# Performance work log

Hardware: AMD Instinct MI355X
Metric: run time of the kernel (lower is better)

## Reference

```python
import jax, jax.numpy as jnp
import numpy as np

# dims: batch, q-heads, kv-heads, seq, head_dim, block size, window (kv blocks per q block)
B, H, KVH, S, D = 2, 16, 4, 4096, 64
BLK, W = 64, 8
G = H // KVH          # heads per group = 4
NQ = S // BLK         # 64 query blocks
L = W * BLK           # flattened kv window per q block = 512


def setup_inputs() -> dict:
    key = jax.random.key(0)
    k0, k1, k2, k3 = jax.random.split(key, 4)
    q = jax.random.normal(k0, (B, H, S, D), jnp.float32)
    k = jax.random.normal(k1, (B, KVH, S, D), jnp.float32)
    v = jax.random.normal(k2, (B, KVH, S, D), jnp.float32)
    # standard alibi slopes 2^(-8i/H)
    alibi_slopes = jnp.asarray(2.0 ** (-8.0 * np.arange(1, H + 1) / H), jnp.float32)
    # contiguous segments via sorted random ids
    segment_ids = jnp.sort(jax.random.randint(k3, (B, S), 0, 8, jnp.int32), axis=-1)
    # causal sliding window: q block qb attends to kv blocks [qb-W+1, qb]; -1 = invalid
    qb = np.arange(NQ)[:, None]
    bi = qb - (W - 1) + np.arange(W)[None, :]
    block_indices = jnp.asarray(np.where(bi < 0, -1, bi), jnp.int32)  # [NQ, W]
    return {"q": q, "k": k, "v": v, "alibi_slopes": alibi_slopes,
            "segment_ids": segment_ids, "block_indices": block_indices}


def reference(q, k, v, alibi_slopes, segment_ids, block_indices):
    scale = jnp.float32(1.0 / np.sqrt(D))
    NEG = jnp.float32(-1e30)

    qg = q.reshape(B, KVH, G, NQ, BLK, D)          # GQA grouping
    kb = k.reshape(B, KVH, NQ, BLK, D)
    vb = v.reshape(B, KVH, NQ, BLK, D)

    safe = jnp.clip(block_indices, 0)               # [NQ, W]
    kg = kb[:, :, safe]                             # [B,KVH,NQ,W,BLK,D] gathered kv blocks
    vg = vb[:, :, safe]

    pos_m = (jnp.arange(NQ) * BLK)[:, None] + jnp.arange(BLK)             # [NQ,BM]
    pos_n = safe[:, :, None] * BLK + jnp.arange(BLK)[None, None, :]       # [NQ,W,BN]

    valid = (block_indices >= 0)[:, None, :, None]                        # [NQ,1,W,1]
    causal = pos_m[:, :, None, None] >= pos_n[:, None, :, :]              # [NQ,BM,W,BN]
    seg_q = segment_ids.reshape(B, NQ, BLK)
    seg_k = jnp.take(segment_ids, pos_n.reshape(-1), axis=1).reshape(B, NQ, W, BLK)
    same_seg = (seg_q[:, :, :, None, None] == seg_k[:, :, None, :, :]) & (seg_q[:, :, :, None, None] >= 0)
    mask = ((valid & causal)[None] & same_seg)                            # [B,NQ,BM,W,BN]
    maskb = mask.reshape(B, 1, 1, NQ, BLK, L)                             # broadcast over KVH,G

    scores = jnp.einsum('bkgqmd,bkqwnd->bkgqmwn', qg, kg) * scale         # [B,KVH,G,NQ,BM,W,BN]
    pos_diff = jnp.abs(pos_m[:, :, None, None] - pos_n[:, None, :, :]).astype(jnp.float32)
    scores = scores - alibi_slopes.reshape(KVH, G)[None, :, :, None, None, None, None] * pos_diff
    scores = scores.reshape(B, KVH, G, NQ, BLK, L)
    scores = jnp.where(maskb, scores, NEG)

    row_max = jnp.max(scores, axis=-1, keepdims=True)
    p = jnp.where(maskb, jnp.exp(scores - row_max), 0.0)
    l = jnp.sum(p, axis=-1, keepdims=True)                                # [B,KVH,G,NQ,BM,1]
    vf = vg.reshape(B, KVH, NQ, L, D)
    acc = jnp.einsum('bkgqml,bkqld->bkgqmd', p, vf)
    out = jnp.where(l > 0, acc / jnp.where(l > 0, l, 1.0), 0.0)           # zero rows with no valid kv
    return out.reshape(B, H, S, D)
```

## Files before the change

kernel.cpp:

```cpp
#include <hip/hip_runtime.h>
#include <hip/hip_bf16.h>

#define NKVH 4
#define SEQ 4096
#define BLK 64
#define NW 8
#define NQB 64

typedef __attribute__((ext_vector_type(8))) short bf16x8;
typedef __attribute__((ext_vector_type(4))) float f32x4;

__device__ __forceinline__ unsigned pkbf(unsigned lo, unsigned hi) {
  return __builtin_amdgcn_perm(hi + 0x8000u, lo + 0x8000u, 0x07060302u);
}

__device__ __forceinline__ void gload16(const void* g, void* l) {
  __builtin_amdgcn_global_load_lds(
      (const __attribute__((address_space(1))) void*)g,
      (__attribute__((address_space(3))) void*)l, 16, 0, 0);
}

__global__ __launch_bounds__(256, 2)
void prep_kernel(const float* __restrict__ kp, const float* __restrict__ vp,
                 const int* __restrict__ seg,
                 short* __restrict__ kw, short* __restrict__ vt,
                 int* __restrict__ fo)
{
  const int ki = blockIdx.x, kvh = blockIdx.y, b = blockIdx.z;
  const size_t base = (((size_t)(b*NKVH + kvh)*SEQ) + (size_t)ki*BLK)*64;
  __shared__ float sk[64][72];
  __shared__ float sv[64][72];
  const int t = threadIdx.x;
  #pragma unroll
  for (int it = 0; it < 4; ++it) {
    const int i = t + it*256;
    const int row = i >> 4, c4 = i & 15;
    float4 a = *(const float4*)(kp + base + row*64 + c4*4);
    *(float4*)&sk[row][c4*4] = a;
    float4 v = *(const float4*)(vp + base + row*64 + c4*4);
    *(float4*)&sv[row][c4*4] = v;
  }
  if (kvh == 0 && t < BLK) {
    const int idx = ki*BLK + t;
    const int v = seg[b*SEQ + idx];
    const bool bnd = (idx == 0) || (seg[b*SEQ + idx - 1] != v);
    if (bnd) fo[b*8 + v] = idx;
  }
  __syncthreads();
  #pragma unroll
  for (int it = 0; it < 2; ++it) {
    const int o = t + it*256;
    const int s = o >> 8, fd = (o >> 6) & 3, lg = (o >> 4) & 3, lr = o & 15;
    const int krow = 8*(lr >> 2) + (lr & 3) + 4*(fd & 1) + 32*(fd >> 1);
    const float* src = &sk[krow][s*32 + lg*8];
    uint4 w;
    w.x = pkbf(__float_as_uint(src[0]), __float_as_uint(src[1]));
    w.y = pkbf(__float_as_uint(src[2]), __float_as_uint(src[3]));
    w.z = pkbf(__float_as_uint(src[4]), __float_as_uint(src[5]));
    w.w = pkbf(__float_as_uint(src[6]), __float_as_uint(src[7]));
    *(uint4*)(kw + base + (size_t)o*8) = w;
    const int d = fd*16 + lr;
    const int n0 = s*32 + lg*8;
    uint4 u;
    u.x = pkbf(__float_as_uint(sv[n0+0][d]), __float_as_uint(sv[n0+1][d]));
    u.y = pkbf(__float_as_uint(sv[n0+2][d]), __float_as_uint(sv[n0+3][d]));
    u.z = pkbf(__float_as_uint(sv[n0+4][d]), __float_as_uint(sv[n0+5][d]));
    u.w = pkbf(__float_as_uint(sv[n0+6][d]), __float_as_uint(sv[n0+7][d]));
    *(uint4*)(vt + base + (size_t)o*8) = u;
  }
}

__global__ __launch_bounds__(256, 2)
void sattn_kernel(const float* __restrict__ qp, const short* __restrict__ kw,
                  const short* __restrict__ vt, const float* __restrict__ alibi,
                  const int* __restrict__ seg, const int* __restrict__ bidx,
                  const int* __restrict__ fo, float* __restrict__ outp)
{
  const int raw = blockIdx.x;
  const int xcd = raw & 7, li = raw >> 3;
  const int b = xcd >> 2, kvh = xcd & 3;
  const int qb = li & 63, hp = li >> 6;

  const int tid = threadIdx.x;
  const int wave = tid >> 6, lane = tid & 63;
  const int lr = lane & 15, lg = lane >> 4;
  const int wh = wave & 1, wq = wave >> 1;
  const int head = kvh*4 + hp*2 + wh;

  __shared__ short klds[2][4096];
  __shared__ short vlds[2][4096];

  int kis[NW];
  #pragma unroll
  for (int i = 0; i < NW; ++i) kis[i] = bidx[qb*NW + i];

  int m_glob[2], lo[2];
  unsigned relm[2];
  #pragma unroll
  for (int g = 0; g < 2; ++g) {
    m_glob[g] = qb*BLK + (wq*2 + g)*16 + lr;
    const int sv = seg[b*SEQ + m_glob[g]];
    lo[g] = fo[b*8 + sv];
    relm[g] = (unsigned)(m_glob[g] - lo[g]);
  }
  const float LOG2E = 1.4426950408889634f;
  const float nslope = -alibi[head] * LOG2E;
  float nsr[4];
  #pragma unroll
  for (int r = 0; r < 4; ++r) nsr[r] = -nslope * (float)r;

  const short* kbase = kw + ((size_t)(b*NKVH + kvh)*SEQ)*64;
  const short* vbase = vt + ((size_t)(b*NKVH + kvh)*SEQ)*64;

  auto STAGE = [&](int buf, int wi) {
    const int ki = kis[wi] < 0 ? 0 : kis[wi];
    const char* ksrc = (const char*)(kbase + (size_t)ki*4096);
    const char* vsrc = (const char*)(vbase + (size_t)ki*4096);
    gload16(ksrc + tid*16,        (char*)&klds[buf][0] + wave*1024);
    gload16(ksrc + 4096 + tid*16, (char*)&klds[buf][0] + 4096 + wave*1024);
    gload16(vsrc + tid*16,        (char*)&vlds[buf][0] + wave*1024);
    gload16(vsrc + 4096 + tid*16, (char*)&vlds[buf][0] + 4096 + wave*1024);
  };

  STAGE(0, 0);

  bf16x8 qf[2][2];
  {
    const float qs = 0.125f * LOG2E;
    #pragma unroll
    for (int g = 0; g < 2; ++g) {
      const float* qrow = qp + (((size_t)b*16 + head)*SEQ + m_glob[g])*64;
      #pragma unroll
      for (int s = 0; s < 2; ++s) {
        float4 a = *(const float4*)(qrow + s*32 + lg*8);
        float4 c = *(const float4*)(qrow + s*32 + lg*8 + 4);
        union { unsigned u[4]; bf16x8 v; } cv;
        cv.u[0] = pkbf(__float_as_uint(a.x*qs), __float_as_uint(a.y*qs));
        cv.u[1] = pkbf(__float_as_uint(a.z*qs), __float_as_uint(a.w*qs));
        cv.u[2] = pkbf(__float_as_uint(c.x*qs), __float_as_uint(c.y*qs));
        cv.u[3] = pkbf(__float_as_uint(c.z*qs), __float_as_uint(c.w*qs));
        qf[g][s] = cv.v;
      }
    }
  }

  union { unsigned short us[8]; bf16x8 v; } one_u;
  #pragma unroll
  for (int i = 0; i < 8; ++i) one_u.us[i] = 0x3F80;
  const bf16x8 onesf = one_u.v;

  f32x4 oacc[2][4], osum[2];
  #pragma unroll
  for (int g = 0; g < 2; ++g) {
    f32x4 z = {0.f,0.f,0.f,0.f};
    osum[g] = z;
    #pragma unroll
    for (int dt = 0; dt < 4; ++dt) oacc[g][dt] = z;
  }

  asm volatile("s_waitcnt vmcnt(0)" ::: "memory");
  __builtin_amdgcn_s_barrier();

  #pragma unroll
  for (int wi = 0; wi < NW; ++wi) {
    const int cur = wi & 1;
    if (wi + 1 < NW) STAGE(cur ^ 1, wi + 1);
    const int kvi = kis[wi];
    if (kvi >= 0) {
      f32x4 sacc[2][4];
      #pragma unroll
      for (int g = 0; g < 2; ++g)
        #pragma unroll
        for (int f = 0; f < 4; ++f) { f32x4 z = {0.f,0.f,0.f,0.f}; sacc[g][f] = z; }
      #pragma unroll
      for (int s = 0; s < 2; ++s) {
        bf16x8 kf[4];
        #pragma unroll
        for (int f = 0; f < 4; ++f)
          kf[f] = *(const bf16x8*)&klds[cur][(s*256 + f*64 + lane)*8];
        __builtin_amdgcn_s_setprio(1);
        #pragma unroll
        for (int f = 0; f < 4; ++f)
          sacc[0][f] = __builtin_amdgcn_mfma_f32_16x16x32_bf16(kf[f], qf[0][s], sacc[0][f], 0, 0, 0);
        #pragma unroll
        for (int f = 0; f < 4; ++f)
          sacc[1][f] = __builtin_amdgcn_mfma_f32_16x16x32_bf16(kf[f], qf[1][s], sacc[1][f], 0, 0, 0);
        __builtin_amdgcn_s_setprio(0);
      }

      unsigned pk[2][4][2];
      #pragma unroll
      for (int g = 0; g < 2; ++g) {
        #pragma unroll
        for (int f = 0; f < 4; ++f) {
          const int nb = lg*8 + 4*(f & 1) + 32*(f >> 1);
          const int n0 = kvi*BLK + nb;
          const unsigned nrel0 = (unsigned)(n0 - lo[g]);
          const float af = nslope * (float)(m_glob[g] - n0);
          float p[4];
          #pragma unroll
          for (int r = 0; r < 4; ++r) {
            const bool live = (nrel0 + (unsigned)r) <= relm[g];
            const float pv = __builtin_amdgcn_exp2f(sacc[g][f][r] + af + nsr[r]);
            p[r] = live ? pv : 0.f;
          }
          pk[g][f][0] = pkbf(__float_as_uint(p[0]), __float_as_uint(p[1]));
          pk[g][f][1] = pkbf(__float_as_uint(p[2]), __float_as_uint(p[3]));
        }
      }

      #pragma unroll
      for (int s = 0; s < 2; ++s) {
        bf16x8 vf[4];
        #pragma unroll
        for (int dt = 0; dt < 4; ++dt)
          vf[dt] = *(const bf16x8*)&vlds[cur][(s*256 + dt*64 + lane)*8];
        union { unsigned u[4]; bf16x8 v; } pf0, pf1;
        pf0.u[0] = pk[0][2*s][0]; pf0.u[1] = pk[0][2*s][1];
        pf0.u[2] = pk[0][2*s+1][0]; pf0.u[3] = pk[0][2*s+1][1];
        pf1.u[0] = pk[1][2*s][0]; pf1.u[1] = pk[1][2*s][1];
        pf1.u[2] = pk[1][2*s+1][0]; pf1.u[3] = pk[1][2*s+1][1];
        __builtin_amdgcn_s_setprio(1);
        #pragma unroll
        for (int dt = 0; dt < 4; ++dt)
          oacc[0][dt] = __builtin_amdgcn_mfma_f32_16x16x32_bf16(vf[dt], pf0.v, oacc[0][dt], 0, 0, 0);
        #pragma unroll
        for (int dt = 0; dt < 4; ++dt)
          oacc[1][dt] = __builtin_amdgcn_mfma_f32_16x16x32_bf16(vf[dt], pf1.v, oacc[1][dt], 0, 0, 0);
        osum[0] = __builtin_amdgcn_mfma_f32_16x16x32_bf16(onesf, pf0.v, osum[0], 0, 0, 0);
        osum[1] = __builtin_amdgcn_mfma_f32_16x16x32_bf16(onesf, pf1.v, osum[1], 0, 0, 0);
        __builtin_amdgcn_s_setprio(0);
      }
    }
    if (wi + 1 < NW) {
      asm volatile("s_waitcnt vmcnt(0)" ::: "memory");
      __builtin_amdgcn_s_barrier();
    }
  }

  #pragma unroll
  for (int g = 0; g < 2; ++g) {
    const float lrow = osum[g][0];
    const float inv = lrow > 0.f ? 1.f/lrow : 0.f;
    float* dst = outp + (((size_t)b*16 + head)*SEQ + m_glob[g])*64;
    #pragma unroll
    for (int dt = 0; dt < 4; ++dt) {
      float4 o;
      o.x = oacc[g][dt][0]*inv; o.y = oacc[g][dt][1]*inv;
      o.z = oacc[g][dt][2]*inv; o.w = oacc[g][dt][3]*inv;
      *(float4*)&dst[dt*16 + lg*4] = o;
    }
  }
}

extern "C" void kernel_launch(void* const* d_in, const int* in_sizes, int n_in,
                              void* d_out, int out_size, void* d_ws, size_t ws_size,
                              hipStream_t stream) {
  const float* q    = (const float*)d_in[0];
  const float* k    = (const float*)d_in[1];
  const float* v    = (const float*)d_in[2];
  const float* al   = (const float*)d_in[3];
  const int*   sg   = (const int*)d_in[4];
  const int*   bi   = (const int*)d_in[5];
  short* kws  = (short*)d_ws;
  short* vtws = (short*)((char*)d_ws + (size_t)(1u<<22));
  int*   fo   = (int*)((char*)d_ws + (size_t)(1u<<23));
  dim3 pgrid(NQB, NKVH, 2);
  prep_kernel<<<pgrid, 256, 0, stream>>>(k, v, sg, kws, vtws, fo);
  sattn_kernel<<<dim3(1024), 256, 0, stream>>>(q, kws, vtws, al, sg, bi, fo, (float*)d_out);
}
```

Before: 46.29 us.

## Stage KV blocks in pairs with 4-deep LDS buffering and prefold ALiBi bias

```diff
diff --git a/kernel.cpp b/kernel.cpp
--- a/kernel.cpp
+++ b/kernel.cpp
@@ -87,8 +87,8 @@
   const int wh = wave & 1, wq = wave >> 1;
   const int head = kvh*4 + hp*2 + wh;
 
-  __shared__ short klds[2][4096];
-  __shared__ short vlds[2][4096];
+  __shared__ short klds[4][4096];
+  __shared__ short vlds[4][4096];
 
   int kis[NW];
   #pragma unroll
@@ -105,9 +105,16 @@
   }
   const float LOG2E = 1.4426950408889634f;
   const float nslope = -alibi[head] * LOG2E;
-  float nsr[4];
-  #pragma unroll
-  for (int r = 0; r < 4; ++r) nsr[r] = -nslope * (float)r;
+
+  float A2[2], cnr[4][4];
+  #pragma unroll
+  for (int g = 0; g < 2; ++g) A2[g] = nslope * (float)m_glob[g];
+  #pragma unroll
+  for (int f = 0; f < 4; ++f) {
+    const int nb = lg*8 + 4*(f & 1) + 32*(f >> 1);
+    #pragma unroll
+    for (int r = 0; r < 4; ++r) cnr[f][r] = nslope * (float)(nb + r);
+  }
 
   const short* kbase = kw + ((size_t)(b*NKVH + kvh)*SEQ)*64;
   const short* vbase = vt + ((size_t)(b*NKVH + kvh)*SEQ)*64;
@@ -123,6 +130,7 @@
   };
 
   STAGE(0, 0);
+  STAGE(1, 1);
 
   bf16x8 qf[2][2];
   {
@@ -162,77 +170,97 @@
   __builtin_amdgcn_s_barrier();
 
   #pragma unroll
-  for (int wi = 0; wi < NW; ++wi) {
-    const int cur = wi & 1;
-    if (wi + 1 < NW) STAGE(cur ^ 1, wi + 1);
-    const int kvi = kis[wi];
-    if (kvi >= 0) {
-      f32x4 sacc[2][4];
-      #pragma unroll
-      for (int g = 0; g < 2; ++g)
+  for (int t2 = 0; t2 < 4; ++t2) {
+    if (t2 < 3) {
+      STAGE((2*t2 + 2) & 3, 2*t2 + 2);
+      STAGE((2*t2 + 3) & 3, 2*t2 + 3);
+    }
+    #pragma unroll
+    for (int w = 0; w < 2; ++w) {
+      const int wi = 2*t2 + w;
+      const int kvi = kis[wi];
+      if (kvi >= 0) {
+        const float B = nslope * (float)(kvi*BLK);
+        const bool fast = (wi != NW-1) &&
+            __all((kvi*BLK >= lo[0]) && (kvi*BLK >= lo[1]));
+
+        f32x4 sacc[2][4];
         #pragma unroll
-        for (int f = 0; f < 4; ++f) { f32x4 z = {0.f,0.f,0.f,0.f}; sacc[g][f] = z; }
-      #pragma unroll
-      for (int s = 0; s < 2; ++s) {
-        bf16x8 kf[4];
+        for (int g = 0; g < 2; ++g) {
+          const float Dg = A2[g] - B;
+          #pragma unroll
+          for (int f = 0; f < 4; ++f)
+            #pragma unroll
+            for (int r = 0; r < 4; ++r) sacc[g][f][r] = Dg - cnr[f][r];
+        }
         #pragma unroll
-        for (int f = 0; f < 4; ++f)
-          kf[f] = *(const bf16x8*)&klds[cur][(s*256 + f*64 + lane)*8];
-        __builtin_amdgcn_s_setprio(1);
+        for (int s = 0; s < 2; ++s) {
+          bf16x8 kf[4];
+          #pragma unroll
+          for (int f = 0; f < 4; ++f)
+            kf[f] = *(const bf16x8*)&klds[wi & 3][(s*256 + f*64 + lane)*8];
+          __builtin_amdgcn_s_setprio(1);
+          #pragma unroll
+          for (int f = 0; f < 4; ++f)
+            sacc[0][f] = __builtin_amdgcn_mfma_f32_16x16x32_bf16(kf[f], qf[0][s], sacc[0][f], 0, 0, 0);
+          #pragma unroll
+          for (int f = 0; f < 4; ++f)
+            sacc[1][f] = __builtin_amdgcn_mfma_f32_16x16x32_bf16(kf[f], qf[1][s], sacc[1][f], 0, 0, 0);
+          __builtin_amdgcn_s_setprio(0);
+        }
+
+        union { unsigned u[4]; bf16x8 v; } pfs[2][2];
+        if (fast) {
+          #pragma unroll
+          for (int g = 0; g < 2; ++g)
+            #pragma unroll
+            for (int f = 0; f < 4; ++f) {
+              const float p0 = __builtin_amdgcn_exp2f(sacc[g][f][0]);
+              const float p1 = __builtin_amdgcn_exp2f(sacc[g][f][1]);
+              const float p2 = __builtin_amdgcn_exp2f(sacc[g][f][2]);
+              const float p3 = __builtin_amdgcn_exp2f(sacc[g][f][3]);
+              pfs[g][f >> 1].u[(f & 1)*2 + 0] = pkbf(__float_as_uint(p0), __float_as_uint(p1));
+              pfs[g][f >> 1].u[(f & 1)*2 + 1] = pkbf(__float_as_uint(p2), __float_as_uint(p3));
+            }
+        } else {
+          #pragma unroll
+          for (int g = 0; g < 2; ++g)
+            #pragma unroll
+            for (int f = 0; f < 4; ++f) {
+              const int nb = lg*8 + 4*(f & 1) + 32*(f >> 1);
+              const unsigned nrel0 = (unsigned)(kvi*BLK + nb - lo[g]);
+              float p[4];
+              #pragma unroll
+              for (int r = 0; r < 4; ++r) {
+                const bool live = (nrel0 + (unsigned)r) <= relm[g];
+                const float pv = __builtin_amdgcn_exp2f(sacc[g][f][r]);
+                p[r] = live ? pv : 0.f;
+              }
+              pfs[g][f >> 1].u[(f & 1)*2 + 0] = pkbf(__float_as_uint(p[0]), __float_as_uint(p[1]));
+              pfs[g][f >> 1].u[(f & 1)*2 + 1] = pkbf(__float_as_uint(p[2]), __float_as_uint(p[3]));
+            }
+        }
+
         #pragma unroll
-        for (int f = 0; f < 4; ++f)
-          sacc[0][f] = __builtin_amdgcn_mfma_f32_16x16x32_bf16(kf[f], qf[0][s], sacc[0][f], 0, 0, 0);
-        #pragma unroll
-        for (int f = 0; f < 4; ++f)
-          sacc[1][f] = __builtin_amdgcn_mfma_f32_16x16x32_bf16(kf[f], qf[1][s], sacc[1][f], 0, 0, 0);
-        __builtin_amdgcn_s_setprio(0);
+        for (int s = 0; s < 2; ++s) {
+          bf16x8 vf[4];
+          #pragma unroll
+          for (int dt = 0; dt < 4; ++dt)
+            vf[dt] = *(const bf16x8*)&vlds[wi & 3][(s*256 + dt*64 + lane)*8];
+          __builtin_amdgcn_s_setprio(1);
+          #pragma unroll
+          for (int dt = 0; dt < 4; ++dt)
+            oacc[0][dt] = __builtin_amdgcn_mfma_f32_16x16x32_bf16(vf[dt], pfs[0][s].v, oacc[0][dt], 0, 0, 0);
+          #pragma unroll
+          for (int dt = 0; dt < 4; ++dt)
+            oacc[1][dt] = __builtin_amdgcn_mfma_f32_16x16x32_bf16(vf[dt], pfs[1][s].v, oacc[1][dt], 0, 0, 0);
+          osum[0] = __builtin_amdgcn_mfma_f32_16x16x32_bf16(onesf, pfs[0][s].v, osum[0], 0, 0, 0);
+          osum[1] = __builtin_amdgcn_mfma_f32_16x16x32_bf16(onesf, pfs[1][s].v, osum[1], 0, 0, 0);
+          __builtin_amdgcn_s_setprio(0);
+        }
       }
-
-      unsigned pk[2][4][2];
-      #pragma unroll
-      for (int g = 0; g < 2; ++g) {
-        #pragma unroll
-        for (int f = 0; f < 4; ++f) {
-          const int nb = lg*8 + 4*(f & 1) + 32*(f >> 1);
-          const int n0 = kvi*BLK + nb;
-          const unsigned nrel0 = (unsigned)(n0 - lo[g]);
-          const float af = nslope * (float)(m_glob[g] - n0);
-          float p[4];
-          #pragma unroll
-          for (int r = 0; r < 4; ++r) {
-            const bool live = (nrel0 + (unsigned)r) <= relm[g];
-            const float pv = __builtin_amdgcn_exp2f(sacc[g][f][r] + af + nsr[r]);
-            p[r] = live ? pv : 0.f;
-          }
-          pk[g][f][0] = pkbf(__float_as_uint(p[0]), __float_as_uint(p[1]));
-          pk[g][f][1] = pkbf(__float_as_uint(p[2]), __float_as_uint(p[3]));
-        }
-      }
-
-      #pragma unroll
-      for (int s = 0; s < 2; ++s) {
-        bf16x8 vf[4];
-        #pragma unroll
-        for (int dt = 0; dt < 4; ++dt)
-          vf[dt] = *(const bf16x8*)&vlds[cur][(s*256 + dt*64 + lane)*8];
-        union { unsigned u[4]; bf16x8 v; } pf0, pf1;
-        pf0.u[0] = pk[0][2*s][0]; pf0.u[1] = pk[0][2*s][1];
-        pf0.u[2] = pk[0][2*s+1][0]; pf0.u[3] = pk[0][2*s+1][1];
-        pf1.u[0] = pk[1][2*s][0]; pf1.u[1] = pk[1][2*s][1];
-        pf1.u[2] = pk[1][2*s+1][0]; pf1.u[3] = pk[1][2*s+1][1];
-        __builtin_amdgcn_s_setprio(1);
-        #pragma unroll
-        for (int dt = 0; dt < 4; ++dt)
-          oacc[0][dt] = __builtin_amdgcn_mfma_f32_16x16x32_bf16(vf[dt], pf0.v, oacc[0][dt], 0, 0, 0);
-        #pragma unroll
-        for (int dt = 0; dt < 4; ++dt)
-          oacc[1][dt] = __builtin_amdgcn_mfma_f32_16x16x32_bf16(vf[dt], pf1.v, oacc[1][dt], 0, 0, 0);
-        osum[0] = __builtin_amdgcn_mfma_f32_16x16x32_bf16(onesf, pf0.v, osum[0], 0, 0, 0);
-        osum[1] = __builtin_amdgcn_mfma_f32_16x16x32_bf16(onesf, pf1.v, osum[1], 0, 0, 0);
-        __builtin_amdgcn_s_setprio(0);
-      }
-    }
-    if (wi + 1 < NW) {
+    }
+    if (t2 < 3) {
       asm volatile("s_waitcnt vmcnt(0)" ::: "memory");
       __builtin_amdgcn_s_barrier();
     }
```

Result: no change. 45.91 us (-0.8%).
